# Optimization experiments

Hardware: AMD Instinct MI355X
Metric: run time of the kernel (lower is better)

The kernel has to match this reference:

```python
import jax, jax.numpy as jnp
import numpy as np

N_DISEASE = 50000
N_GENE = 50000
D = 64
N_EDGES = 2000000

def setup_inputs() -> dict:
    key = jax.random.key(0)
    k1, k2, k3, k4, k5, k6 = jax.random.split(key, 6)
    return {
        "x_disease": jax.random.normal(k1, (N_DISEASE, D), dtype=jnp.float32),
        "h_disease": jax.random.normal(k2, (N_DISEASE, D), dtype=jnp.float32),
        "x_gene": jax.random.normal(k3, (N_GENE, D), dtype=jnp.float32),
        "h_gene": jax.random.normal(k4, (N_GENE, D), dtype=jnp.float32),
        "src": jax.random.randint(k5, (N_EDGES,), 0, N_DISEASE, dtype=jnp.int32),
        "dst": jax.random.randint(k6, (N_EDGES,), 0, N_GENE, dtype=jnp.int32),
    }

def reference(x_disease, h_disease, x_gene, h_gene, src, dst):
    # Concat raw and learned features per node type: [N, 2D]
    f_d = jnp.concatenate([x_disease, h_disease], axis=1)
    f_g = jnp.concatenate([x_gene, h_gene], axis=1)
    # Per-node L2 norms: [N, 1]
    n_d = jnp.linalg.norm(f_d, axis=1, keepdims=True)
    n_g = jnp.linalg.norm(f_g, axis=1, keepdims=True)
    # u_dot_v on features: per-edge gather + dot -> [E, 1]
    dot = jnp.sum(f_d[src] * f_g[dst], axis=1, keepdims=True)
    # u_dot_v on norms (1-dim features): product of norms -> [E, 1]
    mou = n_d[src] * n_g[dst]
    return dot / mou
```

## Files before the change

### kernel.cpp

```cpp
#include <hip/hip_runtime.h>


#define FD 64
#define EDGE_BLOCKS 2048

__device__ __forceinline__ int q8pack(float v0, float v1, float v2, float v3, float inv) {
    float a0 = fminf(fmaxf(v0 * inv, -127.f), 127.f);
    float a1 = fminf(fmaxf(v1 * inv, -127.f), 127.f);
    float a2 = fminf(fmaxf(v2 * inv, -127.f), 127.f);
    float a3 = fminf(fmaxf(v3 * inv, -127.f), 127.f);
    int q0 = ((int)rintf(a0)) & 0xff;
    int q1 = ((int)rintf(a1)) & 0xff;
    int q2 = ((int)rintf(a2)) & 0xff;
    int q3 = ((int)rintf(a3)) & 0xff;
    return q0 | (q1 << 8) | (q2 << 16) | (q3 << 24);
}

__global__ __launch_bounds__(256, 8)
void pack_kernel(const float4* __restrict__ xd, const float4* __restrict__ hd,
                 const float4* __restrict__ xg, const float4* __restrict__ hg,
                 int4* __restrict__ fd, int4* __restrict__ fg,
                 float* __restrict__ sd, float* __restrict__ sg,
                 int n_d, int n_g)
{
    int tid  = (int)(blockIdx.x * blockDim.x + threadIdx.x);
    int node = tid >> 3;
    int lane = threadIdx.x & 7;
    int total = n_d + n_g;
    if (node >= total) return;

    const float4* x; const float4* h; int4* o; float* s; int n;
    if (node < n_d) { x = xd; h = hd; o = fd; s = sd; n = node; }
    else            { x = xg; h = hg; o = fg; s = sg; n = node - n_d; }

    float4 a0 = x[(size_t)n * 16 + lane * 2];
    float4 a1 = x[(size_t)n * 16 + lane * 2 + 1];
    float4 b0 = h[(size_t)n * 16 + lane * 2];
    float4 b1 = h[(size_t)n * 16 + lane * 2 + 1];

    float ss = a0.x*a0.x + a0.y*a0.y + a0.z*a0.z + a0.w*a0.w
             + a1.x*a1.x + a1.y*a1.y + a1.z*a1.z + a1.w*a1.w
             + b0.x*b0.x + b0.y*b0.y + b0.z*b0.z + b0.w*b0.w
             + b1.x*b1.x + b1.y*b1.y + b1.z*b1.z + b1.w*b1.w;
    #pragma unroll
    for (int m = 4; m >= 1; m >>= 1) ss += __shfl_xor(ss, m);
    float r = rsqrtf(ss);

    a0.x *= r; a0.y *= r; a0.z *= r; a0.w *= r;
    a1.x *= r; a1.y *= r; a1.z *= r; a1.w *= r;
    b0.x *= r; b0.y *= r; b0.z *= r; b0.w *= r;
    b1.x *= r; b1.y *= r; b1.z *= r; b1.w *= r;

    float mx = fmaxf(
        fmaxf(fmaxf(fmaxf(fabsf(a0.x), fabsf(a0.y)), fmaxf(fabsf(a0.z), fabsf(a0.w))),
              fmaxf(fmaxf(fabsf(a1.x), fabsf(a1.y)), fmaxf(fabsf(a1.z), fabsf(a1.w)))),
        fmaxf(fmaxf(fmaxf(fabsf(b0.x), fabsf(b0.y)), fmaxf(fabsf(b0.z), fabsf(b0.w))),
              fmaxf(fmaxf(fabsf(b1.x), fabsf(b1.y)), fmaxf(fabsf(b1.z), fabsf(b1.w)))));
    #pragma unroll
    for (int m = 4; m >= 1; m >>= 1) mx = fmaxf(mx, __shfl_xor(mx, m));

    float inv = 127.0f / mx;

    int4 w;
    w.x = q8pack(a0.x, a0.y, a0.z, a0.w, inv);
    w.y = q8pack(a1.x, a1.y, a1.z, a1.w, inv);
    w.z = q8pack(b0.x, b0.y, b0.z, b0.w, inv);
    w.w = q8pack(b1.x, b1.y, b1.z, b1.w, inv);
    o[(size_t)n * 8 + lane] = w;

    if (lane == 0) s[n] = mx * (1.0f / 127.0f);
}

__device__ __forceinline__ int dot4(int a, int b, int c) {
    return __builtin_amdgcn_sdot4(a, b, c, false);
}

__device__ __forceinline__ void edge_pair(const int4* __restrict__ fd,
                                          const int4* __restrict__ fg,
                                          const float* __restrict__ sd,
                                          const float* __restrict__ sg,
                                          const int* __restrict__ src,
                                          const int* __restrict__ dst,
                                          float* __restrict__ out,
                                          int pair, int n_edges, int lane)
{
    int e0 = pair * 2;
    bool has1 = (e0 + 1) < n_edges;

    int s0, d0, s1, d1;
    if (has1) {
        int2 sp = ((const int2*)src)[pair];
        int2 dp = ((const int2*)dst)[pair];
        s0 = sp.x; s1 = sp.y; d0 = dp.x; d1 = dp.y;
    } else {
        s0 = src[e0]; d0 = dst[e0]; s1 = s0; d1 = d0;
    }

    int4 a0 = fd[(size_t)s0 * 8 + lane];
    int4 b0 = fg[(size_t)d0 * 8 + lane];
    int4 a1 = fd[(size_t)s1 * 8 + lane];
    int4 b1 = fg[(size_t)d1 * 8 + lane];

    int acc0 = dot4(a0.x, b0.x, dot4(a0.y, b0.y, dot4(a0.z, b0.z, dot4(a0.w, b0.w, 0))));
    int acc1 = dot4(a1.x, b1.x, dot4(a1.y, b1.y, dot4(a1.z, b1.z, dot4(a1.w, b1.w, 0))));

    acc0 += __shfl_xor(acc0, 4);
    acc0 += __shfl_xor(acc0, 2);
    acc0 += __shfl_xor(acc0, 1);
    acc1 += __shfl_xor(acc1, 4);
    acc1 += __shfl_xor(acc1, 2);
    acc1 += __shfl_xor(acc1, 1);

    if (lane == 0) {
        out[e0] = (float)acc0 * sd[s0] * sg[d0];
        if (has1) out[e0 + 1] = (float)acc1 * sd[s1] * sg[d1];
    }
}

__global__ __launch_bounds__(256, 8)
void edge_kernel4(const int4* __restrict__ fd, const int4* __restrict__ fg,
                  const float* __restrict__ sd, const float* __restrict__ sg,
                  const int* __restrict__ src, const int* __restrict__ dst,
                  float* __restrict__ out, int n_edges, int ngroups)
{
    int g    = (int)blockIdx.x * 32 + (threadIdx.x >> 3);
    int lane = threadIdx.x & 7;
    int npairs = (n_edges + 1) >> 1;

    int pair = g;
    for (; pair + ngroups < npairs; pair += 2 * ngroups) {
        edge_pair(fd, fg, sd, sg, src, dst, out, pair,           n_edges, lane);
        edge_pair(fd, fg, sd, sg, src, dst, out, pair + ngroups, n_edges, lane);
    }
    if (pair < npairs)
        edge_pair(fd, fg, sd, sg, src, dst, out, pair, n_edges, lane);
}

extern "C" void kernel_launch(void* const* d_in, const int* in_sizes, int n_in,
                              void* d_out, int out_size, void* d_ws, size_t ws_size,
                              hipStream_t stream) {
    const float* xd = (const float*)d_in[0];
    const float* hd = (const float*)d_in[1];
    const float* xg = (const float*)d_in[2];
    const float* hg = (const float*)d_in[3];
    const int*  src = (const int*)d_in[4];
    const int*  dst = (const int*)d_in[5];

    int n_d     = in_sizes[0] / FD;
    int n_g     = in_sizes[2] / FD;
    int n_edges = in_sizes[4];

    char* ws = (char*)d_ws;
    int4*  fd = (int4*)ws;   ws += (size_t)n_d * 128;
    int4*  fg = (int4*)ws;   ws += (size_t)n_g * 128;
    float* sd = (float*)ws;  ws += (size_t)n_d * sizeof(float);
    float* sg = (float*)ws;
    float* out = (float*)d_out;

    int total_nodes = n_d + n_g;
    int nb1 = (total_nodes * 8 + 255) / 256;
    pack_kernel<<<nb1, 256, 0, stream>>>((const float4*)xd, (const float4*)hd,
                                         (const float4*)xg, (const float4*)hg,
                                         fd, fg, sd, sg, n_d, n_g);

    long long npairs = ((long long)n_edges + 1) / 2;
    int nb2 = (int)((npairs + 31) / 32);
    if (nb2 > EDGE_BLOCKS) nb2 = EDGE_BLOCKS;
    if (nb2 < 1) nb2 = 1;
    int ngroups = nb2 * 32;
    edge_kernel4<<<nb2, 256, 0, stream>>>(fd, fg, sd, sg, src, dst,
                                          out, n_edges, ngroups);
}
```

Before: 164.2 us.

## Replace grid-stride edge loop with one-pair-per-group grid and shuffled index loads

The edge kernel drops the capped grid-stride loop and launches one block per 32 edge pairs, so each 8-lane group handles exactly one pair. Per wavefront, 16 lanes do one coalesced int2 load each of the src and dst indices and broadcast them with shuffles, instead of every lane in a group reloading the same index. The two results are written as one float2 store. The cost is many more blocks (about 31k versus 2048) and no loop to overlap successive gathers within a thread.

```diff
diff --git a/kernel.cpp b/kernel.cpp
--- a/kernel.cpp
+++ b/kernel.cpp
@@ -2,7 +2,6 @@
 
 
 #define FD 64
-#define EDGE_BLOCKS 2048
 
 __device__ __forceinline__ int q8pack(float v0, float v1, float v2, float v3, float inv) {
     float a0 = fminf(fmaxf(v0 * inv, -127.f), 127.f);
@@ -75,26 +74,43 @@
     return __builtin_amdgcn_sdot4(a, b, c, false);
 }
 
-__device__ __forceinline__ void edge_pair(const int4* __restrict__ fd,
-                                          const int4* __restrict__ fg,
-                                          const float* __restrict__ sd,
-                                          const float* __restrict__ sg,
-                                          const int* __restrict__ src,
-                                          const int* __restrict__ dst,
-                                          float* __restrict__ out,
-                                          int pair, int n_edges, int lane)
+__global__ __launch_bounds__(256, 8)
+void edge_kernel5(const int4* __restrict__ fd, const int4* __restrict__ fg,
+                  const float* __restrict__ sd, const float* __restrict__ sg,
+                  const int* __restrict__ src, const int* __restrict__ dst,
+                  float* __restrict__ out, int n_edges)
 {
+    int npairs = (n_edges + 1) >> 1;
+    int wl   = threadIdx.x & 63;
+    int wid  = threadIdx.x >> 6;
+    int gw   = wl >> 3;
+    int lane = wl & 7;
+    int wavebase = (int)blockIdx.x * 32 + wid * 8;
+
+    int2 r = make_int2(0, 0);
+    if (wl < 16) {
+        int pl = wavebase + (wl & 7);
+        if (pl < npairs) {
+            if ((n_edges & 1) && (pl == npairs - 1)) {
+                int v = (wl < 8) ? src[pl * 2] : dst[pl * 2];
+                r = make_int2(v, v);
+            } else {
+                r = (wl < 8) ? ((const int2*)src)[pl]
+                             : ((const int2*)dst)[pl];
+            }
+        }
+    }
+
+    int pair = wavebase + gw;
+    if (pair >= npairs) return;
     int e0 = pair * 2;
     bool has1 = (e0 + 1) < n_edges;
 
-    int s0, d0, s1, d1;
-    if (has1) {
-        int2 sp = ((const int2*)src)[pair];
-        int2 dp = ((const int2*)dst)[pair];
-        s0 = sp.x; s1 = sp.y; d0 = dp.x; d1 = dp.y;
-    } else {
-        s0 = src[e0]; d0 = dst[e0]; s1 = s0; d1 = d0;
-    }
+    int s0 = __shfl(r.x, gw);
+    int s1 = __shfl(r.y, gw);
+    int d0 = __shfl(r.x, 8 + gw);
+    int d1 = __shfl(r.y, 8 + gw);
+    if (!has1) { s1 = s0; d1 = d0; }
 
     int4 a0 = fd[(size_t)s0 * 8 + lane];
     int4 b0 = fg[(size_t)d0 * 8 + lane];
@@ -112,28 +128,14 @@
     acc1 += __shfl_xor(acc1, 1);
 
     if (lane == 0) {
-        out[e0] = (float)acc0 * sd[s0] * sg[d0];
-        if (has1) out[e0 + 1] = (float)acc1 * sd[s1] * sg[d1];
+        float r0 = (float)acc0 * sd[s0] * sg[d0];
+        if (has1) {
+            float r1 = (float)acc1 * sd[s1] * sg[d1];
+            ((float2*)out)[pair] = make_float2(r0, r1);
+        } else {
+            out[e0] = r0;
+        }
     }
-}
-
-__global__ __launch_bounds__(256, 8)
-void edge_kernel4(const int4* __restrict__ fd, const int4* __restrict__ fg,
-                  const float* __restrict__ sd, const float* __restrict__ sg,
-                  const int* __restrict__ src, const int* __restrict__ dst,
-                  float* __restrict__ out, int n_edges, int ngroups)
-{
-    int g    = (int)blockIdx.x * 32 + (threadIdx.x >> 3);
-    int lane = threadIdx.x & 7;
-    int npairs = (n_edges + 1) >> 1;
-
-    int pair = g;
-    for (; pair + ngroups < npairs; pair += 2 * ngroups) {
-        edge_pair(fd, fg, sd, sg, src, dst, out, pair,           n_edges, lane);
-        edge_pair(fd, fg, sd, sg, src, dst, out, pair + ngroups, n_edges, lane);
-    }
-    if (pair < npairs)
-        edge_pair(fd, fg, sd, sg, src, dst, out, pair, n_edges, lane);
 }
 
 extern "C" void kernel_launch(void* const* d_in, const int* in_sizes, int n_in,
@@ -163,11 +165,9 @@
                                          (const float4*)xg, (const float4*)hg,
                                          fd, fg, sd, sg, n_d, n_g);
 
-    long long npairs = ((long long)n_edges + 1) / 2;
-    int nb2 = (int)((npairs + 31) / 32);
-    if (nb2 > EDGE_BLOCKS) nb2 = EDGE_BLOCKS;
+    int npairs = (n_edges + 1) / 2;
+    int nb2 = (npairs + 31) / 32;
     if (nb2 < 1) nb2 = 1;
-    int ngroups = nb2 * 32;
-    edge_kernel4<<<nb2, 256, 0, stream>>>(fd, fg, sd, sg, src, dst,
-                                          out, n_edges, ngroups);
+    edge_kernel5<<<nb2, 256, 0, stream>>>(fd, fg, sd, sg, src, dst,
+                                          out, n_edges);
 }
```

Result: faster. 158.4 us (-3.5%).
